# Performance work log

Measured on AMD Instinct MI355X. Metric: run time of the kernel, lower is better.

The kernel has to match this reference:

```python
import jax, jax.numpy as jnp
import numpy as np

T, D_IN, NE = 131072, 1024, 64

def setup_inputs() -> dict:
    key = jax.random.key(0)
    k1, k2 = jax.random.split(key)
    x = jax.random.normal(k1, (T, D_IN), dtype=jnp.float32)
    W = jax.random.normal(k2, (NE, D_IN), dtype=jnp.float32) * (1.0 / np.sqrt(D_IN))
    return {"x": x, "W": W, "top_k": 2}

def reference(x, W, top_k):
    # fp32 router logits: [T, Ne]
    logits = jnp.einsum('td,ed->te', x.astype(jnp.float32), W.astype(jnp.float32))
    k = min(int(top_k), W.shape[0])
    vals, idx = jax.lax.top_k(logits, k)           # [T, k] each
    w = jax.nn.softmax(vals, axis=-1).astype(x.dtype)
    return (idx, w)
```

## Files before the change

### kernel.cpp

```cpp
#include <hip/hip_runtime.h>
#include <math.h>

constexpr int T_TOKENS = 131072;
constexpr int D        = 1024;
constexpr float EPS_GAP = 1e-3f;

typedef __attribute__((ext_vector_type(8))) short bf16x8;
typedef __attribute__((ext_vector_type(4))) float f32x4;
typedef __bf16 bf16v8 __attribute__((ext_vector_type(8)));
typedef float  f32v8  __attribute__((ext_vector_type(8)));

__device__ __forceinline__ void split2(const float4 lo, const float4 hi,
                                       bf16x8& p0, bf16x8& p1) {
    f32v8 f = {lo.x, lo.y, lo.z, lo.w, hi.x, hi.y, hi.z, hi.w};
    bf16v8 h0 = __builtin_convertvector(f, bf16v8);
    f32v8 back = __builtin_convertvector(h0, f32v8);
    bf16v8 h1 = __builtin_convertvector(f - back, bf16v8);
    p0 = __builtin_bit_cast(bf16x8, h0);
    p1 = __builtin_bit_cast(bf16x8, h1);
}

__global__ void prep_w(const float* __restrict__ W, bf16x8* __restrict__ wpl) {
    const int g = blockIdx.x;
    const int c = threadIdx.x >> 6;
    const int l = threadIdx.x & 63;
    const int e  = c * 16 + (l & 15);
    const int k0 = g * 32 + (l >> 4) * 8;
    const float4 lo = *(const float4*)(W + (long)e * D + k0);
    const float4 hi = *(const float4*)(W + (long)e * D + k0 + 4);
    bf16x8 p0, p1; split2(lo, hi, p0, p1);
    const int base = ((g * 4 + c) * 2) * 64 + l;
    wpl[base]      = p0;
    wpl[base + 64] = p1;
}

__global__ __launch_bounds__(256, 4)
void router_mfma(const float* __restrict__ x, const bf16x8* __restrict__ wpl,
                 float* __restrict__ out, unsigned* __restrict__ wcnt,
                 unsigned* __restrict__ wlist, unsigned cap)
{
    __shared__ __align__(16) char Xs[4][2][4096];

    const int tid = threadIdx.x;
    const int wv  = tid >> 6;
    const int l   = tid & 63;
    const int lg  = l >> 4;
    const int lr  = l & 15;
    const long t0 = (long)blockIdx.x * 128 + wv * 32;
    const int swz = (lr & 7) << 4;
    const char* xb = (const char*)x;

    f32x4 acc[2][4];
#pragma unroll
    for (int a = 0; a < 2; ++a)
#pragma unroll
        for (int c = 0; c < 4; ++c) acc[a][c] = f32x4{0.f, 0.f, 0.f, 0.f};

#define STAGE(S, BUF)                                                          \
    {                                                                          \
        _Pragma("unroll")                                                      \
        for (int i = 0; i < 4; ++i) {                                          \
            const int rr = 8 * i + (l >> 3);                                   \
            const char* src = xb + (t0 + rr) * 4096L + (S) * 128               \
                              + (((l & 7) * 16) ^ ((rr & 7) << 4));            \
            char* dst = &Xs[wv][BUF][i * 1024];                                \
            __builtin_amdgcn_global_load_lds(                                  \
                (const __attribute__((address_space(1))) void*)src,            \
                (__attribute__((address_space(3))) void*)dst, 16, 0, 0);       \
        }                                                                      \
    }

    STAGE(0, 0);

#pragma unroll 1
    for (int s = 0; s < 32; ++s) {
        const int buf = s & 1;
        bf16x8 w[8];
#pragma unroll
        for (int q = 0; q < 8; ++q)
            w[q] = wpl[(size_t)s * 512 + q * 64 + l];
        const int sn = (s + 1 < 32) ? s + 1 : 31;
        if (buf) { STAGE(sn, 0) } else { STAGE(sn, 1) }
        asm volatile("s_waitcnt vmcnt(12)" ::: "memory");
        __builtin_amdgcn_sched_barrier(0);
        const char* ab = &Xs[wv][buf][0];
#pragma unroll
        for (int a = 0; a < 2; ++a) {
            const char* rowp = ab + (a * 16 + lr) * 128;
            const int c0 = lg * 32;
            const float4 lo = *(const float4*)(rowp + (c0 ^ swz));
            const float4 hi = *(const float4*)(rowp + ((c0 + 16) ^ swz));
            bf16x8 a0, a1;
            split2(lo, hi, a0, a1);
#pragma unroll
            for (int c = 0; c < 4; ++c) {
                acc[a][c] = __builtin_amdgcn_mfma_f32_16x16x32_bf16(a0, w[c*2+0], acc[a][c], 0, 0, 0);
                acc[a][c] = __builtin_amdgcn_mfma_f32_16x16x32_bf16(a1, w[c*2+0], acc[a][c], 0, 0, 0);
                acc[a][c] = __builtin_amdgcn_mfma_f32_16x16x32_bf16(a0, w[c*2+1], acc[a][c], 0, 0, 0);
            }
        }
    }
#undef STAGE

#pragma unroll
    for (int a = 0; a < 2; ++a)
#pragma unroll
    for (int r = 0; r < 4; ++r) {
        float v1 = acc[a][0][r]; int i1 = lr;
        float v2 = -INFINITY;    int i2 = 1 << 20;
        float v3 = -INFINITY;
#pragma unroll
        for (int c = 1; c < 4; ++c) {
            const float v = acc[a][c][r]; const int e = lr + 16 * c;
            if (v > v1)      { v3 = v2; v2 = v1; i2 = i1; v1 = v; i1 = e; }
            else if (v > v2) { v3 = v2; v2 = v;  i2 = e; }
            else if (v > v3) { v3 = v; }
        }
#pragma unroll
        for (int m = 8; m >= 1; m >>= 1) {
            const float ov1 = __shfl_xor(v1, m);
            const int   oi1 = __shfl_xor(i1, m);
            const float ov2 = __shfl_xor(v2, m);
            const int   oi2 = __shfl_xor(i2, m);
            const float ov3 = __shfl_xor(v3, m);
            const bool tv = v1 >= ov1;
            const float x2 = tv ? v2 : ov2, x3 = tv ? v3 : ov3;
            const float y1 = tv ? ov1 : v1, y2 = tv ? ov2 : v2;
            const float nv3 = (x2 >= y1) ? fmaxf(x3, y1) : fmaxf(x2, y2);
            const bool aw = (ov1 > v1) || (ov1 == v1 && oi1 < i1);
            const float nv1 = aw ? ov1 : v1; const int ni1 = aw ? oi1 : i1;
            const float c1v = aw ? v1  : ov1; const int c1i = aw ? i1  : oi1;
            const float c2v = aw ? ov2 : v2;  const int c2i = aw ? oi2 : i2;
            const bool bw = (c1v > c2v) || (c1v == c2v && c1i < c2i);
            v1 = nv1; i1 = ni1;
            v2 = bw ? c1v : c2v; i2 = bw ? c1i : c2i;
            v3 = nv3;
        }
        if (lr == 0) {
            const long t = t0 + a * 16 + lg * 4 + r;
            const float e  = expf(v2 - v1);
            const float dn = 1.0f + e;
            out[t * 2 + 0] = (float)i1;
            out[t * 2 + 1] = (float)i2;
            out[(long)T_TOKENS * 2 + t * 2 + 0] = 1.0f / dn;
            out[(long)T_TOKENS * 2 + t * 2 + 1] = e / dn;
            if (v1 - v2 < EPS_GAP || v2 - v3 < EPS_GAP) {
                const unsigned p = atomicAdd(wcnt, 1u);
                if (p < cap) wlist[p] = (unsigned)t;
            }
        }
    }
}

__global__ __launch_bounds__(256)
void router_fixup(const float* __restrict__ x, const float* __restrict__ W,
                  float* __restrict__ out, const unsigned* __restrict__ wcnt,
                  const unsigned* __restrict__ wlist, unsigned cap)
{
    __shared__ float ps[4][64];
    unsigned cnt = wcnt[0]; if (cnt > cap) cnt = cap;
    const int wv = threadIdx.x >> 6;
    const int l  = threadIdx.x & 63;
    const int kb = (wv == 0) ? 0 : (wv == 1) ? 320 : (wv == 2) ? 640 : 832;
    const int ke = (wv == 0) ? 320 : (wv == 1) ? 640 : (wv == 2) ? 832 : 1024;

    for (unsigned it = blockIdx.x; it < cnt; it += gridDim.x) {
        const long t = (long)wlist[it];
        const float* xr = x + t * (long)D;
        const float* wr = W + (long)l * D;
        float accP = 0.f;
#pragma unroll 4
        for (int k = kb; k < ke; k += 4) {
            const float4 xv = *(const float4*)(xr + k);
            const float4 wvv = *(const float4*)(wr + k);
            accP = fmaf(xv.x, wvv.x, accP);
            accP = fmaf(xv.y, wvv.y, accP);
            accP = fmaf(xv.z, wvv.z, accP);
            accP = fmaf(xv.w, wvv.w, accP);
        }
        ps[wv][l] = accP;
        __syncthreads();
        if (wv == 0) {
            const float accT = __fadd_rn(__fadd_rn(__fadd_rn(ps[0][l], ps[1][l]), ps[2][l]), ps[3][l]);
            float v1 = accT; int i1 = l;
            float v2 = -INFINITY; int i2 = 1 << 20;
#pragma unroll
            for (int m = 32; m >= 1; m >>= 1) {
                const float ov1 = __shfl_xor(v1, m);
                const int   oi1 = __shfl_xor(i1, m);
                const float ov2 = __shfl_xor(v2, m);
                const int   oi2 = __shfl_xor(i2, m);
                const bool aw = (ov1 > v1) || (ov1 == v1 && oi1 < i1);
                const float nv1 = aw ? ov1 : v1; const int ni1 = aw ? oi1 : i1;
                const float c1v = aw ? v1  : ov1; const int c1i = aw ? i1  : oi1;
                const float c2v = aw ? ov2 : v2;  const int c2i = aw ? oi2 : i2;
                const bool bw = (c1v > c2v) || (c1v == c2v && c1i < c2i);
                v1 = nv1; i1 = ni1;
                v2 = bw ? c1v : c2v; i2 = bw ? c1i : c2i;
            }
            if (l == 0) {
                const float e  = expf(v2 - v1);
                const float dn = 1.0f + e;
                out[t * 2 + 0] = (float)i1;
                out[t * 2 + 1] = (float)i2;
                out[(long)T_TOKENS * 2 + t * 2 + 0] = 1.0f / dn;
                out[(long)T_TOKENS * 2 + t * 2 + 1] = e / dn;
            }
        }
        __syncthreads();
    }
}

extern "C" void kernel_launch(void* const* d_in, const int* in_sizes, int n_in,
                              void* d_out, int out_size, void* d_ws, size_t ws_size,
                              hipStream_t stream) {
    const float* x = (const float*)d_in[0];
    const float* W = (const float*)d_in[1];
    float* out = (float*)d_out;

    unsigned* wcnt  = (unsigned*)d_ws;
    bf16x8*   wpl   = (bf16x8*)((char*)d_ws + 1024);
    unsigned* wlist = (unsigned*)((char*)d_ws + 1024 + 262144);
    size_t rem = (ws_size - 1024 - 262144) / 4;
    unsigned cap = (unsigned)(rem > (1u << 22) ? (1u << 22) : rem);

    (void)hipMemsetAsync(d_ws, 0, 64, stream);
    prep_w<<<dim3(32), dim3(256), 0, stream>>>(W, wpl);
    router_mfma<<<dim3(T_TOKENS / 128), dim3(256), 0, stream>>>(x, wpl, out, wcnt, wlist, cap);
    router_fixup<<<dim3(512), dim3(256), 0, stream>>>(x, W, out, wcnt, wlist, cap);
}
```

Baseline: 196.4 us.

## Split K across waves with LDS reduction, 16 tokens per block

Each block now handles 16 tokens, and its four waves each cover a quarter of the D dimension (split-K) instead of each wave streaming all of K for 32 tokens. All x data for the block is loaded into LDS in one shot, then partial accumulators are reduced through LDS by wave 0, which runs the top-k epilogue. This gives many more, shorter blocks and removes the serial double-buffered K loop. The costs are a sync, an LDS reduction, three of four waves idling during the epilogue, and more total loading of the W-plane per token, since every block rereads all of W.

```diff
diff --git a/kernel.cpp b/kernel.cpp
--- a/kernel.cpp
+++ b/kernel.cpp
@@ -34,84 +34,84 @@
     wpl[base + 64] = p1;
 }
 
-__global__ __launch_bounds__(256, 4)
+__global__ __launch_bounds__(256, 2)
 void router_mfma(const float* __restrict__ x, const bf16x8* __restrict__ wpl,
                  float* __restrict__ out, unsigned* __restrict__ wcnt,
                  unsigned* __restrict__ wlist, unsigned cap)
 {
-    __shared__ __align__(16) char Xs[4][2][4096];
+    __shared__ __align__(16) char lds[4][16][1024];
 
     const int tid = threadIdx.x;
     const int wv  = tid >> 6;
     const int l   = tid & 63;
     const int lg  = l >> 4;
     const int lr  = l & 15;
-    const long t0 = (long)blockIdx.x * 128 + wv * 32;
+    const long t0 = (long)blockIdx.x * 16;
     const int swz = (lr & 7) << 4;
     const char* xb = (const char*)x;
 
-    f32x4 acc[2][4];
-#pragma unroll
-    for (int a = 0; a < 2; ++a)
-#pragma unroll
-        for (int c = 0; c < 4; ++c) acc[a][c] = f32x4{0.f, 0.f, 0.f, 0.f};
-
-#define STAGE(S, BUF)                                                          \
-    {                                                                          \
-        _Pragma("unroll")                                                      \
-        for (int i = 0; i < 4; ++i) {                                          \
-            const int rr = 8 * i + (l >> 3);                                   \
-            const char* src = xb + (t0 + rr) * 4096L + (S) * 128               \
-                              + (((l & 7) * 16) ^ ((rr & 7) << 4));            \
-            char* dst = &Xs[wv][BUF][i * 1024];                                \
-            __builtin_amdgcn_global_load_lds(                                  \
-                (const __attribute__((address_space(1))) void*)src,            \
-                (__attribute__((address_space(3))) void*)dst, 16, 0, 0);       \
-        }                                                                      \
-    }
-
-    STAGE(0, 0);
-
-#pragma unroll 1
-    for (int s = 0; s < 32; ++s) {
-        const int buf = s & 1;
+#pragma unroll
+    for (int i = 0; i < 16; ++i) {
+        const char* src = xb + (t0 + i) * 4096L + wv * 1024
+                          + ((l * 16) ^ ((i & 7) << 4));
+        char* dst = &lds[wv][i][0];
+        __builtin_amdgcn_global_load_lds(
+            (const __attribute__((address_space(1))) void*)src,
+            (__attribute__((address_space(3))) void*)dst, 16, 0, 0);
+    }
+    asm volatile("s_waitcnt vmcnt(0)" ::: "memory");
+    __builtin_amdgcn_sched_barrier(0);
+
+    f32x4 acc[4];
+#pragma unroll
+    for (int c = 0; c < 4; ++c) acc[c] = f32x4{0.f, 0.f, 0.f, 0.f};
+
+#pragma unroll
+    for (int kk = 0; kk < 8; ++kk) {
+        const int g = wv * 8 + kk;
         bf16x8 w[8];
 #pragma unroll
         for (int q = 0; q < 8; ++q)
-            w[q] = wpl[(size_t)s * 512 + q * 64 + l];
-        const int sn = (s + 1 < 32) ? s + 1 : 31;
-        if (buf) { STAGE(sn, 0) } else { STAGE(sn, 1) }
-        asm volatile("s_waitcnt vmcnt(12)" ::: "memory");
-        __builtin_amdgcn_sched_barrier(0);
-        const char* ab = &Xs[wv][buf][0];
-#pragma unroll
-        for (int a = 0; a < 2; ++a) {
-            const char* rowp = ab + (a * 16 + lr) * 128;
-            const int c0 = lg * 32;
-            const float4 lo = *(const float4*)(rowp + (c0 ^ swz));
-            const float4 hi = *(const float4*)(rowp + ((c0 + 16) ^ swz));
-            bf16x8 a0, a1;
-            split2(lo, hi, a0, a1);
-#pragma unroll
-            for (int c = 0; c < 4; ++c) {
-                acc[a][c] = __builtin_amdgcn_mfma_f32_16x16x32_bf16(a0, w[c*2+0], acc[a][c], 0, 0, 0);
-                acc[a][c] = __builtin_amdgcn_mfma_f32_16x16x32_bf16(a1, w[c*2+0], acc[a][c], 0, 0, 0);
-                acc[a][c] = __builtin_amdgcn_mfma_f32_16x16x32_bf16(a0, w[c*2+1], acc[a][c], 0, 0, 0);
-            }
-        }
-    }
-#undef STAGE
-
-#pragma unroll
-    for (int a = 0; a < 2; ++a)
+            w[q] = wpl[(size_t)g * 512 + q * 64 + l];
+        const char* rowp = &lds[wv][lr][0];
+        const int c0 = kk * 128 + lg * 32;
+        const float4 lo = *(const float4*)(rowp + (c0 ^ swz));
+        const float4 hi = *(const float4*)(rowp + ((c0 + 16) ^ swz));
+        bf16x8 a0, a1;
+        split2(lo, hi, a0, a1);
+#pragma unroll
+        for (int c = 0; c < 4; ++c) {
+            acc[c] = __builtin_amdgcn_mfma_f32_16x16x32_bf16(a0, w[c*2+0], acc[c], 0, 0, 0);
+            acc[c] = __builtin_amdgcn_mfma_f32_16x16x32_bf16(a1, w[c*2+0], acc[c], 0, 0, 0);
+            acc[c] = __builtin_amdgcn_mfma_f32_16x16x32_bf16(a0, w[c*2+1], acc[c], 0, 0, 0);
+        }
+    }
+
+    {
+        char* pw = &lds[wv][0][0];
+#pragma unroll
+        for (int c = 0; c < 4; ++c)
+            *(f32x4*)(pw + l * 64 + c * 16) = acc[c];
+    }
+    __syncthreads();
+    if (wv != 0) return;
+
+#pragma unroll
+    for (int w2 = 1; w2 < 4; ++w2) {
+        const char* pr = &lds[w2][0][0];
+#pragma unroll
+        for (int c = 0; c < 4; ++c)
+            acc[c] += *(const f32x4*)(pr + l * 64 + c * 16);
+    }
+
 #pragma unroll
     for (int r = 0; r < 4; ++r) {
-        float v1 = acc[a][0][r]; int i1 = lr;
-        float v2 = -INFINITY;    int i2 = 1 << 20;
+        float v1 = acc[0][r]; int i1 = lr;
+        float v2 = -INFINITY; int i2 = 1 << 20;
         float v3 = -INFINITY;
 #pragma unroll
         for (int c = 1; c < 4; ++c) {
-            const float v = acc[a][c][r]; const int e = lr + 16 * c;
+            const float v = acc[c][r]; const int e = lr + 16 * c;
             if (v > v1)      { v3 = v2; v2 = v1; i2 = i1; v1 = v; i1 = e; }
             else if (v > v2) { v3 = v2; v2 = v;  i2 = e; }
             else if (v > v3) { v3 = v; }
@@ -137,7 +137,7 @@
             v3 = nv3;
         }
         if (lr == 0) {
-            const long t = t0 + a * 16 + lg * 4 + r;
+            const long t = t0 + lg * 4 + r;
             const float e  = expf(v2 - v1);
             const float dn = 1.0f + e;
             out[t * 2 + 0] = (float)i1;
@@ -226,6 +226,6 @@
 
     (void)hipMemsetAsync(d_ws, 0, 64, stream);
     prep_w<<<dim3(32), dim3(256), 0, stream>>>(W, wpl);
-    router_mfma<<<dim3(T_TOKENS / 128), dim3(256), 0, stream>>>(x, wpl, out, wcnt, wlist, cap);
+    router_mfma<<<dim3(T_TOKENS / 16), dim3(256), 0, stream>>>(x, wpl, out, wcnt, wlist, cap);
     router_fixup<<<dim3(512), dim3(256), 0, stream>>>(x, W, out, wcnt, wlist, cap);
 }
```

Result: slower. 295.1 us (+50.2%).
